# Kernel optimization log

Hardware: AMD Instinct MI355X
Metric: run time of the kernel (lower is better)

The kernel has to match this reference:

```python
import jax, jax.numpy as jnp
import numpy as np

NUM_HEAD = 8
DIM_MODEL = 512
DIM_HEAD = DIM_MODEL // NUM_HEAD
LN_EPS = 1e-5


def setup_inputs() -> dict:
    key = jax.random.key(0)
    ks = jax.random.split(key, 12)
    B, L, D = 4, 2048, DIM_MODEL
    s = 0.02
    return {
        "x": jax.random.normal(ks[0], (B, L, D), dtype=jnp.float32),
        "Wq": jax.random.normal(ks[1], (D, D), dtype=jnp.float32) * s,
        "bq": jnp.zeros((D,), dtype=jnp.float32),
        "Wk": jax.random.normal(ks[2], (D, D), dtype=jnp.float32) * s,
        "bk": jnp.zeros((D,), dtype=jnp.float32),
        "Wv": jax.random.normal(ks[3], (D, D), dtype=jnp.float32) * s,
        "bv": jnp.zeros((D,), dtype=jnp.float32),
        "Wo": jax.random.normal(ks[4], (D, D), dtype=jnp.float32) * s,
        "bo": jnp.zeros((D,), dtype=jnp.float32),
        "gamma": jnp.ones((D,), dtype=jnp.float32),
        "beta": jnp.zeros((D,), dtype=jnp.float32),
    }


def reference(x, Wq, bq, Wk, bk, Wv, bv, Wo, bo, gamma, beta):
    B, L, D = x.shape
    H, dh = NUM_HEAD, D // NUM_HEAD
    # QKV projections (torch Linear: x @ W.T + b)
    Q = x @ Wq.T + bq
    K = x @ Wk.T + bk
    V = x @ Wv.T + bv
    # Faithful to the torch code: contiguous view(B*H, L, dh)
    Q = Q.reshape(B * H, L, dh)
    K = K.reshape(B * H, L, dh)
    V = V.reshape(B * H, L, dh)
    scale = dh ** (-0.5)
    # [B*H, L, L] scores, scaled, softmax over keys
    attn = jax.nn.softmax(jnp.einsum("bqd,bkd->bqk", Q, K) * scale, axis=-1)
    context = jnp.einsum("bqk,bkd->bqd", attn, V)  # [B*H, L, dh]
    context = context.reshape(B, L, D)
    out = context @ Wo.T + bo
    out = out + x  # residual (dropout p=0.0 -> identity)
    # LayerNorm over last dim
    mu = jnp.mean(out, axis=-1, keepdims=True)
    var = jnp.mean(jnp.square(out - mu), axis=-1, keepdims=True)
    out = (out - mu) / jnp.sqrt(var + LN_EPS) * gamma + beta
    return out
```

## Files before the change

### kernel.cpp

```cpp
#include <hip/hip_runtime.h>

typedef __bf16 bf16;
typedef __bf16 bf16x4 __attribute__((ext_vector_type(4)));
typedef __bf16 bf16x8 __attribute__((ext_vector_type(8)));
typedef float f32x4 __attribute__((ext_vector_type(4)));
typedef float f32x16 __attribute__((ext_vector_type(16)));
typedef unsigned int u32;

#define MFMA16(A, B, C) __builtin_amdgcn_mfma_f32_16x16x32_bf16((A), (B), (C), 0, 0, 0)
#define MFMA32(A, B, C) __builtin_amdgcn_mfma_f32_32x32x16_bf16((A), (B), (C), 0, 0, 0)

constexpr int Dm   = 512;
constexpr int Lm   = 2048;
constexpr int DH   = 64;
constexpr int Mrows = 8192;
constexpr int NHEADS = 32;

__device__ __forceinline__ void gload16(const void* g, void* l) {
    __builtin_amdgcn_global_load_lds(
        (const __attribute__((address_space(1))) void*)g,
        (__attribute__((address_space(3))) void*)l, 16, 0, 0);
}

__device__ __forceinline__ u32 pack2(float a, float b) {
    unsigned short la = __builtin_bit_cast(unsigned short, (bf16)a);
    unsigned short lb = __builtin_bit_cast(unsigned short, (bf16)b);
    return (u32)la | ((u32)lb << 16);
}

__global__ __launch_bounds__(256)
void cvt_kernel(const float* __restrict__ x, const float* __restrict__ Wq,
                const float* __restrict__ Wk, const float* __restrict__ Wv,
                const float* __restrict__ Wo,
                bf16* __restrict__ xb, bf16* __restrict__ Wqb, bf16* __restrict__ Wkb,
                bf16* __restrict__ Wvb, bf16* __restrict__ Wob)
{
    size_t i = ((size_t)blockIdx.x * 256 + threadIdx.x) * 4;
    const float* src; bf16* dst; size_t off;
    if (i < (size_t)Mrows * Dm) {
        src = x; dst = xb; off = i;
    } else {
        size_t r = i - (size_t)Mrows * Dm;
        int w = (int)(r >> 18);
        off = r & 262143;
        src = (w == 0) ? Wq : (w == 1) ? Wk : (w == 2) ? Wv : Wo;
        dst = (w == 0) ? Wqb : (w == 1) ? Wkb : (w == 2) ? Wvb : Wob;
    }
    float4 v = *reinterpret_cast<const float4*>(src + off);
    bf16x4 o; o[0] = (bf16)v.x; o[1] = (bf16)v.y; o[2] = (bf16)v.z; o[3] = (bf16)v.w;
    *reinterpret_cast<bf16x4*>(dst + off) = o;
}

__global__ __launch_bounds__(256)
void qkv_gemm(const bf16* __restrict__ xb,
              const bf16* __restrict__ Wqb, const float* __restrict__ bq,
              const bf16* __restrict__ Wkb, const float* __restrict__ bk,
              const bf16* __restrict__ Wvb, const float* __restrict__ bv,
              bf16* __restrict__ Qo, bf16* __restrict__ Ko, bf16* __restrict__ Vo)
{
    __shared__ bf16 Asm[128 * 64];
    __shared__ bf16 Bsm[128 * 64];

    const int z = blockIdx.z;
    const bf16* W = (z == 0) ? Wqb : (z == 1) ? Wkb : Wvb;
    const float* bias = (z == 0) ? bq : (z == 1) ? bk : bv;
    bf16* out = (z == 0) ? Qo : (z == 1) ? Ko : Vo;

    const int tid = threadIdx.x;
    const int row0 = blockIdx.y * 128;
    const int col0 = blockIdx.x * 128;

    const int wv = tid >> 6;
    const int ln = tid & 63;
    const int wr = wv >> 1, wc = wv & 1;
    const int lr = ln & 15;
    const int lg = ln >> 4;

    const int srow_b = wv * 8 + (ln >> 3);
    const int ssc = ((ln & 7) ^ (ln >> 3)) * 8;

    f32x4 acc[4][4] = {};

    for (int kt = 0; kt < Dm; kt += 64) {
        __syncthreads();
        #pragma unroll
        for (int j = 0; j < 4; ++j) {
            const int row = j * 32 + srow_b;
            const int base = (j * 256 + wv * 64) * 8;
            gload16(xb + (size_t)(row0 + row) * Dm + kt + ssc, &Asm[base]);
            gload16(W + (size_t)(col0 + row) * Dm + kt + ssc, &Bsm[base]);
        }
        __syncthreads();

        #pragma unroll
        for (int ks = 0; ks < 2; ++ks) {
            bf16x8 af[4], bfv[4];
            #pragma unroll
            for (int m = 0; m < 4; ++m) {
                const int R = wr * 64 + m * 16 + lr;
                af[m] = *reinterpret_cast<const bf16x8*>(&Asm[R * 64 + (((ks * 4 + lg) ^ (R & 7)) * 8)]);
            }
            #pragma unroll
            for (int n = 0; n < 4; ++n) {
                const int R = wc * 64 + n * 16 + lr;
                bfv[n] = *reinterpret_cast<const bf16x8*>(&Bsm[R * 64 + (((ks * 4 + lg) ^ (R & 7)) * 8)]);
            }
            #pragma unroll
            for (int m = 0; m < 4; ++m)
                #pragma unroll
                for (int n = 0; n < 4; ++n)
                    acc[m][n] = MFMA16(af[m], bfv[n], acc[m][n]);
        }
    }

    #pragma unroll
    for (int m = 0; m < 4; ++m)
        #pragma unroll
        for (int n = 0; n < 4; ++n)
            #pragma unroll
            for (int i = 0; i < 4; ++i) {
                int r = row0 + wr * 64 + m * 16 + lg * 4 + i;
                int c = col0 + wc * 64 + n * 16 + lr;
                out[(size_t)r * Dm + c] = (bf16)(acc[m][n][i] + bias[c]);
            }
}

__global__ __launch_bounds__(256)
void oproj_gemm(const bf16* __restrict__ ctx, const bf16* __restrict__ Wob,
                const float* __restrict__ bo, const float* __restrict__ x,
                float* __restrict__ tmp)
{
    __shared__ bf16 Asm[128 * 64];
    __shared__ bf16 Bsm[128 * 64];

    const int tid = threadIdx.x;
    const int row0 = blockIdx.y * 128;
    const int col0 = blockIdx.x * 128;

    const int wv = tid >> 6;
    const int ln = tid & 63;
    const int wr = wv >> 1, wc = wv & 1;
    const int lr = ln & 15;
    const int lg = ln >> 4;

    const int srow_b = wv * 8 + (ln >> 3);
    const int ssc = ((ln & 7) ^ (ln >> 3)) * 8;

    f32x4 acc[4][4] = {};

    for (int kt = 0; kt < Dm; kt += 64) {
        __syncthreads();
        #pragma unroll
        for (int j = 0; j < 4; ++j) {
            const int row = j * 32 + srow_b;
            const int base = (j * 256 + wv * 64) * 8;
            gload16(ctx + (size_t)(row0 + row) * Dm + kt + ssc, &Asm[base]);
            gload16(Wob + (size_t)(col0 + row) * Dm + kt + ssc, &Bsm[base]);
        }
        __syncthreads();

        #pragma unroll
        for (int ks = 0; ks < 2; ++ks) {
            bf16x8 af[4], bfv[4];
            #pragma unroll
            for (int m = 0; m < 4; ++m) {
                const int R = wr * 64 + m * 16 + lr;
                af[m] = *reinterpret_cast<const bf16x8*>(&Asm[R * 64 + (((ks * 4 + lg) ^ (R & 7)) * 8)]);
            }
            #pragma unroll
            for (int n = 0; n < 4; ++n) {
                const int R = wc * 64 + n * 16 + lr;
                bfv[n] = *reinterpret_cast<const bf16x8*>(&Bsm[R * 64 + (((ks * 4 + lg) ^ (R & 7)) * 8)]);
            }
            #pragma unroll
            for (int m = 0; m < 4; ++m)
                #pragma unroll
                for (int n = 0; n < 4; ++n)
                    acc[m][n] = MFMA16(af[m], bfv[n], acc[m][n]);
        }
    }

    #pragma unroll
    for (int m = 0; m < 4; ++m)
        #pragma unroll
        for (int n = 0; n < 4; ++n)
            #pragma unroll
            for (int i = 0; i < 4; ++i) {
                int r = row0 + wr * 64 + m * 16 + lg * 4 + i;
                int c = col0 + wc * 64 + n * 16 + lr;
                tmp[(size_t)r * Dm + c] = acc[m][n][i] + bo[c] + x[(size_t)r * Dm + c];
            }
}

__global__ __launch_bounds__(256)
void vt_kernel(const bf16* __restrict__ V, bf16* __restrict__ Vt)
{
    __shared__ bf16 T[64 * 72];
    const int head = blockIdx.y;
    const int k0 = blockIdx.x * 64;
    const size_t hb = (size_t)head * (Lm * DH);
    const int tid = threadIdx.x;
    const int r = tid >> 2;
    const int seg = (tid & 3) * 16;

    {
        const bf16* src = &V[hb + (size_t)(k0 + r) * DH + seg];
        *reinterpret_cast<bf16x8*>(&T[r * 72 + seg])     = reinterpret_cast<const bf16x8*>(src)[0];
        *reinterpret_cast<bf16x8*>(&T[r * 72 + seg + 8]) = reinterpret_cast<const bf16x8*>(src)[1];
    }
    __syncthreads();
    bf16 o[16];
    #pragma unroll
    for (int j = 0; j < 16; ++j) o[j] = T[(seg + j) * 72 + r];
    *reinterpret_cast<bf16x8*>(&Vt[hb + (size_t)r * Lm + k0 + seg])     = *reinterpret_cast<bf16x8*>(&o[0]);
    *reinterpret_cast<bf16x8*>(&Vt[hb + (size_t)r * Lm + k0 + seg + 8]) = *reinterpret_cast<bf16x8*>(&o[8]);
}

__global__ __launch_bounds__(512)
void flash_attn(const bf16* __restrict__ Q, const bf16* __restrict__ K,
                const bf16* __restrict__ Vt, bf16* __restrict__ ctx)
{
    __shared__ bf16 Ksm[2][64 * 76];
    __shared__ bf16 Vsm[2][64 * 76];

    const int head = blockIdx.y;
    const int q0 = blockIdx.x * 256;
    const size_t hb = (size_t)head * (Lm * DH);

    const int tid = threadIdx.x;
    const int wv = tid >> 6;
    const int ln = tid & 63;
    const int q31 = ln & 31;
    const int hi = ln >> 5;

    const int srow = tid >> 3;
    const int scu  = tid & 7;
    const int sb = srow * 76 + scu * 8;

    const int qrow = q0 + wv * 32 + q31;

    const float qscale = 0.125f * 1.44269504088896340736f;
    bf16x8 qf[4];
    #pragma unroll
    for (int c = 0; c < 4; ++c) {
        bf16x8 t = *reinterpret_cast<const bf16x8*>(&Q[hb + (size_t)qrow * DH + c * 16 + hi * 8]);
        #pragma unroll
        for (int j = 0; j < 8; ++j) qf[c][j] = (bf16)((float)t[j] * qscale);
    }

    f32x16 acc0 = {};
    f32x16 acc1 = {};
    float lsum = 0.f;

    const bf16* Kp = &K[hb + (size_t)srow * DH + scu * 8];
    const bf16* Vp = &Vt[hb + (size_t)srow * Lm + scu * 8];

    bf16x8 kreg = *reinterpret_cast<const bf16x8*>(Kp);
    bf16x8 vreg = *reinterpret_cast<const bf16x8*>(Vp);
    *reinterpret_cast<bf16x8*>(&Ksm[0][sb]) = kreg;
    *reinterpret_cast<bf16x8*>(&Vsm[0][sb]) = vreg;
    kreg = *reinterpret_cast<const bf16x8*>(Kp + 64 * DH);
    vreg = *reinterpret_cast<const bf16x8*>(Vp + 64);
    __syncthreads();

    constexpr int NT = Lm / 64;
    for (int t = 0; t < NT; ++t) {
        const int cur = t & 1;
        if (t + 1 < NT) {
            *reinterpret_cast<bf16x8*>(&Ksm[cur ^ 1][sb]) = kreg;
            *reinterpret_cast<bf16x8*>(&Vsm[cur ^ 1][sb]) = vreg;
        }
        if (t + 2 < NT) {
            kreg = *reinterpret_cast<const bf16x8*>(Kp + (size_t)(t + 2) * 64 * DH);
            vreg = *reinterpret_cast<const bf16x8*>(Vp + (t + 2) * 64);
        }

        #pragma unroll
        for (int kb = 0; kb < 2; ++kb) {
            f32x16 s = {};
            __builtin_amdgcn_s_setprio(1);
            #pragma unroll
            for (int c = 0; c < 4; ++c) {
                bf16x8 kf = *reinterpret_cast<const bf16x8*>(
                    &Ksm[cur][(kb * 32 + q31) * 76 + (c * 2 + hi) * 8]);
                s = MFMA32(kf, qf[c], s);
            }
            __builtin_amdgcn_s_setprio(0);

            float p[16];
            #pragma unroll
            for (int r = 0; r < 16; ++r) { p[r] = exp2f(s[r]); lsum += p[r]; }

            u32 pk_[8], xk[8];
            #pragma unroll
            for (int r = 0; r < 8; ++r) pk_[r] = pack2(p[2 * r], p[2 * r + 1]);
            #pragma unroll
            for (int r = 0; r < 8; ++r) xk[r] = (u32)__shfl_xor((int)pk_[r], 32);

            union PFrag { u32 w[4]; bf16x8 v; } f0, f1;
            f0.w[0] = hi ? xk[2] : pk_[0];
            f0.w[1] = hi ? xk[3] : pk_[1];
            f0.w[2] = hi ? pk_[2] : xk[0];
            f0.w[3] = hi ? pk_[3] : xk[1];
            f1.w[0] = hi ? xk[6] : pk_[4];
            f1.w[1] = hi ? xk[7] : pk_[5];
            f1.w[2] = hi ? pk_[6] : xk[4];
            f1.w[3] = hi ? pk_[7] : xk[5];

            __builtin_amdgcn_s_setprio(1);
            {
                bf16x8 v00 = *reinterpret_cast<const bf16x8*>(
                    &Vsm[cur][(q31) * 76 + (kb * 4 + hi) * 8]);
                acc0 = MFMA32(v00, f0.v, acc0);
                bf16x8 v01 = *reinterpret_cast<const bf16x8*>(
                    &Vsm[cur][(q31) * 76 + (kb * 4 + 2 + hi) * 8]);
                acc0 = MFMA32(v01, f1.v, acc0);
                bf16x8 v10 = *reinterpret_cast<const bf16x8*>(
                    &Vsm[cur][(32 + q31) * 76 + (kb * 4 + hi) * 8]);
                acc1 = MFMA32(v10, f0.v, acc1);
                bf16x8 v11 = *reinterpret_cast<const bf16x8*>(
                    &Vsm[cur][(32 + q31) * 76 + (kb * 4 + 2 + hi) * 8]);
                acc1 = MFMA32(v11, f1.v, acc1);
            }
            __builtin_amdgcn_s_setprio(0);
        }

        __syncthreads();
    }

    lsum += __shfl_xor(lsum, 32);
    const float inv = 1.f / lsum;

    #pragma unroll
    for (int g8 = 0; g8 < 4; ++g8) {
        bf16x4 o0, o1;
        #pragma unroll
        for (int i = 0; i < 4; ++i) {
            o0[i] = (bf16)(acc0[g8 * 4 + i] * inv);
            o1[i] = (bf16)(acc1[g8 * 4 + i] * inv);
        }
        const int d0 = g8 * 8 + hi * 4;
        *reinterpret_cast<bf16x4*>(&ctx[hb + (size_t)qrow * DH + d0])      = o0;
        *reinterpret_cast<bf16x4*>(&ctx[hb + (size_t)qrow * DH + 32 + d0]) = o1;
    }
}

__global__ __launch_bounds__(128)
void ln_kernel(const float* __restrict__ tmp, const float* __restrict__ gamma,
               const float* __restrict__ beta, float* __restrict__ out)
{
    const int row = blockIdx.x;
    const int tid = threadIdx.x;
    const int wv = tid >> 6;
    const int ln = tid & 63;

    float4 v = reinterpret_cast<const float4*>(tmp + (size_t)row * Dm)[tid];
    float s = v.x + v.y + v.z + v.w;
    float sq = v.x * v.x + v.y * v.y + v.z * v.z + v.w * v.w;

    #pragma unroll
    for (int off = 32; off > 0; off >>= 1) {
        s += __shfl_down(s, off);
        sq += __shfl_down(sq, off);
    }
    __shared__ float red[4];
    if (ln == 0) { red[wv * 2] = s; red[wv * 2 + 1] = sq; }
    __syncthreads();
    s = red[0] + red[2];
    sq = red[1] + red[3];

    const float mu = s * (1.f / Dm);
    const float var = sq * (1.f / Dm) - mu * mu;
    const float rstd = rsqrtf(var + 1e-5f);

    float4 g = reinterpret_cast<const float4*>(gamma)[tid];
    float4 b = reinterpret_cast<const float4*>(beta)[tid];
    float4 o;
    o.x = (v.x - mu) * rstd * g.x + b.x;
    o.y = (v.y - mu) * rstd * g.y + b.y;
    o.z = (v.z - mu) * rstd * g.z + b.z;
    o.w = (v.w - mu) * rstd * g.w + b.w;
    reinterpret_cast<float4*>(out + (size_t)row * Dm)[tid] = o;
}

extern "C" void kernel_launch(void* const* d_in, const int* in_sizes, int n_in,
                              void* d_out, int out_size, void* d_ws, size_t ws_size,
                              hipStream_t stream)
{
    const float* x  = (const float*)d_in[0];
    const float* Wq = (const float*)d_in[1];
    const float* bq = (const float*)d_in[2];
    const float* Wk = (const float*)d_in[3];
    const float* bk = (const float*)d_in[4];
    const float* Wv = (const float*)d_in[5];
    const float* bv = (const float*)d_in[6];
    const float* Wo = (const float*)d_in[7];
    const float* bo = (const float*)d_in[8];
    const float* gamma = (const float*)d_in[9];
    const float* beta  = (const float*)d_in[10];
    float* out = (float*)d_out;

    const size_t MD = (size_t)Mrows * Dm;
    const size_t WD = (size_t)Dm * Dm;
    char* p = (char*)d_ws;
    bf16* xb  = (bf16*)p;                 p += MD * 2;
    bf16* Qw  = (bf16*)p;                 p += MD * 2;
    bf16* Kw  = (bf16*)p;                 p += MD * 2;
    bf16* Vw  = (bf16*)p;                 p += MD * 2;
    bf16* Vtw = (bf16*)p;                 p += MD * 2;
    bf16* Wqb = (bf16*)p;                 p += WD * 2;
    bf16* Wkb = (bf16*)p;                 p += WD * 2;
    bf16* Wvb = (bf16*)p;                 p += WD * 2;
    bf16* Wob = (bf16*)p;                 p += WD * 2;
    float* Tw = (float*)d_ws;
    bf16* Cw = Vw;

    {
        const size_t total = MD + 4 * WD;
        cvt_kernel<<<dim3((unsigned)(total / (256 * 4))), 256, 0, stream>>>(
            x, Wq, Wk, Wv, Wo, xb, Wqb, Wkb, Wvb, Wob);
    }

    qkv_gemm<<<dim3(Dm / 128, Mrows / 128, 3), 256, 0, stream>>>(
        xb, Wqb, bq, Wkb, bk, Wvb, bv, Qw, Kw, Vw);

    vt_kernel<<<dim3(Lm / 64, NHEADS), 256, 0, stream>>>(Vw, Vtw);

    flash_attn<<<dim3(Lm / 256, NHEADS), 512, 0, stream>>>(Qw, Kw, Vtw, Cw);

    oproj_gemm<<<dim3(Dm / 128, Mrows / 128), 256, 0, stream>>>(Cw, Wob, bo, x, Tw);

    ln_kernel<<<dim3(Mrows), 128, 0, stream>>>(Tw, gamma, beta, out);
}
```

Measured before the change: 202.0 us.

## Shrink flash attention blocks, use permlane32 swap, and unroll both key halves

```diff
diff --git a/kernel.cpp b/kernel.cpp
--- a/kernel.cpp
+++ b/kernel.cpp
@@ -26,6 +26,10 @@
     unsigned short la = __builtin_bit_cast(unsigned short, (bf16)a);
     unsigned short lb = __builtin_bit_cast(unsigned short, (bf16)b);
     return (u32)la | ((u32)lb << 16);
+}
+
+__device__ __forceinline__ void pl32swap(u32& a, u32& b) {
+    asm("v_permlane32_swap_b32 %0, %1" : "+v"(a), "+v"(b));
 }
 
 __global__ __launch_bounds__(256)
@@ -216,7 +220,7 @@
     *reinterpret_cast<bf16x8*>(&Vt[hb + (size_t)r * Lm + k0 + seg + 8]) = *reinterpret_cast<bf16x8*>(&o[8]);
 }
 
-__global__ __launch_bounds__(512)
+__global__ __launch_bounds__(256, 2)
 void flash_attn(const bf16* __restrict__ Q, const bf16* __restrict__ K,
                 const bf16* __restrict__ Vt, bf16* __restrict__ ctx)
 {
@@ -224,7 +228,7 @@
     __shared__ bf16 Vsm[2][64 * 76];
 
     const int head = blockIdx.y;
-    const int q0 = blockIdx.x * 256;
+    const int q0 = blockIdx.x * 128;
     const size_t hb = (size_t)head * (Lm * DH);
 
     const int tid = threadIdx.x;
@@ -233,9 +237,9 @@
     const int q31 = ln & 31;
     const int hi = ln >> 5;
 
-    const int srow = tid >> 3;
-    const int scu  = tid & 7;
-    const int sb = srow * 76 + scu * 8;
+    const int srow = tid >> 2;
+    const int scu  = tid & 3;
+    const int sb   = srow * 76 + scu * 8;
 
     const int qrow = q0 + wv * 32 + q31;
 
@@ -255,75 +259,90 @@
     const bf16* Kp = &K[hb + (size_t)srow * DH + scu * 8];
     const bf16* Vp = &Vt[hb + (size_t)srow * Lm + scu * 8];
 
-    bf16x8 kreg = *reinterpret_cast<const bf16x8*>(Kp);
-    bf16x8 vreg = *reinterpret_cast<const bf16x8*>(Vp);
-    *reinterpret_cast<bf16x8*>(&Ksm[0][sb]) = kreg;
-    *reinterpret_cast<bf16x8*>(&Vsm[0][sb]) = vreg;
-    kreg = *reinterpret_cast<const bf16x8*>(Kp + 64 * DH);
-    vreg = *reinterpret_cast<const bf16x8*>(Vp + 64);
+    bf16x8 kr0 = *reinterpret_cast<const bf16x8*>(Kp);
+    bf16x8 kr1 = *reinterpret_cast<const bf16x8*>(Kp + 32);
+    bf16x8 vr0 = *reinterpret_cast<const bf16x8*>(Vp);
+    bf16x8 vr1 = *reinterpret_cast<const bf16x8*>(Vp + 32);
+    *reinterpret_cast<bf16x8*>(&Ksm[0][sb])      = kr0;
+    *reinterpret_cast<bf16x8*>(&Ksm[0][sb + 32]) = kr1;
+    *reinterpret_cast<bf16x8*>(&Vsm[0][sb])      = vr0;
+    *reinterpret_cast<bf16x8*>(&Vsm[0][sb + 32]) = vr1;
+    kr0 = *reinterpret_cast<const bf16x8*>(Kp + 64 * DH);
+    kr1 = *reinterpret_cast<const bf16x8*>(Kp + 64 * DH + 32);
+    vr0 = *reinterpret_cast<const bf16x8*>(Vp + 64);
+    vr1 = *reinterpret_cast<const bf16x8*>(Vp + 64 + 32);
     __syncthreads();
 
     constexpr int NT = Lm / 64;
     for (int t = 0; t < NT; ++t) {
         const int cur = t & 1;
         if (t + 1 < NT) {
-            *reinterpret_cast<bf16x8*>(&Ksm[cur ^ 1][sb]) = kreg;
-            *reinterpret_cast<bf16x8*>(&Vsm[cur ^ 1][sb]) = vreg;
+            *reinterpret_cast<bf16x8*>(&Ksm[cur ^ 1][sb])      = kr0;
+            *reinterpret_cast<bf16x8*>(&Ksm[cur ^ 1][sb + 32]) = kr1;
+            *reinterpret_cast<bf16x8*>(&Vsm[cur ^ 1][sb])      = vr0;
+            *reinterpret_cast<bf16x8*>(&Vsm[cur ^ 1][sb + 32]) = vr1;
         }
         if (t + 2 < NT) {
-            kreg = *reinterpret_cast<const bf16x8*>(Kp + (size_t)(t + 2) * 64 * DH);
-            vreg = *reinterpret_cast<const bf16x8*>(Vp + (t + 2) * 64);
-        }
-
-        #pragma unroll
-        for (int kb = 0; kb < 2; ++kb) {
-            f32x16 s = {};
-            __builtin_amdgcn_s_setprio(1);
-            #pragma unroll
-            for (int c = 0; c < 4; ++c) {
-                bf16x8 kf = *reinterpret_cast<const bf16x8*>(
-                    &Ksm[cur][(kb * 32 + q31) * 76 + (c * 2 + hi) * 8]);
-                s = MFMA32(kf, qf[c], s);
-            }
-            __builtin_amdgcn_s_setprio(0);
-
-            float p[16];
-            #pragma unroll
-            for (int r = 0; r < 16; ++r) { p[r] = exp2f(s[r]); lsum += p[r]; }
-
-            u32 pk_[8], xk[8];
-            #pragma unroll
-            for (int r = 0; r < 8; ++r) pk_[r] = pack2(p[2 * r], p[2 * r + 1]);
-            #pragma unroll
-            for (int r = 0; r < 8; ++r) xk[r] = (u32)__shfl_xor((int)pk_[r], 32);
-
-            union PFrag { u32 w[4]; bf16x8 v; } f0, f1;
-            f0.w[0] = hi ? xk[2] : pk_[0];
-            f0.w[1] = hi ? xk[3] : pk_[1];
-            f0.w[2] = hi ? pk_[2] : xk[0];
-            f0.w[3] = hi ? pk_[3] : xk[1];
-            f1.w[0] = hi ? xk[6] : pk_[4];
-            f1.w[1] = hi ? xk[7] : pk_[5];
-            f1.w[2] = hi ? pk_[6] : xk[4];
-            f1.w[3] = hi ? pk_[7] : xk[5];
-
-            __builtin_amdgcn_s_setprio(1);
-            {
-                bf16x8 v00 = *reinterpret_cast<const bf16x8*>(
-                    &Vsm[cur][(q31) * 76 + (kb * 4 + hi) * 8]);
-                acc0 = MFMA32(v00, f0.v, acc0);
-                bf16x8 v01 = *reinterpret_cast<const bf16x8*>(
-                    &Vsm[cur][(q31) * 76 + (kb * 4 + 2 + hi) * 8]);
-                acc0 = MFMA32(v01, f1.v, acc0);
-                bf16x8 v10 = *reinterpret_cast<const bf16x8*>(
-                    &Vsm[cur][(32 + q31) * 76 + (kb * 4 + hi) * 8]);
-                acc1 = MFMA32(v10, f0.v, acc1);
-                bf16x8 v11 = *reinterpret_cast<const bf16x8*>(
-                    &Vsm[cur][(32 + q31) * 76 + (kb * 4 + 2 + hi) * 8]);
-                acc1 = MFMA32(v11, f1.v, acc1);
-            }
-            __builtin_amdgcn_s_setprio(0);
-        }
+            kr0 = *reinterpret_cast<const bf16x8*>(Kp + (size_t)(t + 2) * 64 * DH);
+            kr1 = *reinterpret_cast<const bf16x8*>(Kp + (size_t)(t + 2) * 64 * DH + 32);
+            vr0 = *reinterpret_cast<const bf16x8*>(Vp + (t + 2) * 64);
+            vr1 = *reinterpret_cast<const bf16x8*>(Vp + (t + 2) * 64 + 32);
+        }
+
+        f32x16 s0 = {}, s1 = {};
+        __builtin_amdgcn_s_setprio(1);
+        #pragma unroll
+        for (int c = 0; c < 4; ++c) {
+            bf16x8 k0 = *reinterpret_cast<const bf16x8*>(&Ksm[cur][(q31) * 76 + (c * 2 + hi) * 8]);
+            s0 = MFMA32(k0, qf[c], s0);
+            bf16x8 k1 = *reinterpret_cast<const bf16x8*>(&Ksm[cur][(32 + q31) * 76 + (c * 2 + hi) * 8]);
+            s1 = MFMA32(k1, qf[c], s1);
+        }
+        __builtin_amdgcn_s_setprio(0);
+
+        float p0[16], p1[16];
+        #pragma unroll
+        for (int r = 0; r < 16; ++r) { p0[r] = exp2f(s0[r]); lsum += p0[r]; }
+        #pragma unroll
+        for (int r = 0; r < 16; ++r) { p1[r] = exp2f(s1[r]); lsum += p1[r]; }
+
+        u32 a0[8], a1[8];
+        #pragma unroll
+        for (int r = 0; r < 8; ++r) a0[r] = pack2(p0[2 * r], p0[2 * r + 1]);
+        #pragma unroll
+        for (int r = 0; r < 8; ++r) a1[r] = pack2(p1[2 * r], p1[2 * r + 1]);
+        pl32swap(a0[0], a0[2]); pl32swap(a0[1], a0[3]);
+        pl32swap(a0[4], a0[6]); pl32swap(a0[5], a0[7]);
+        pl32swap(a1[0], a1[2]); pl32swap(a1[1], a1[3]);
+        pl32swap(a1[4], a1[6]); pl32swap(a1[5], a1[7]);
+
+        union PF { u32 w[4]; bf16x8 v; } f0, f1, f2, f3;
+        f0.w[0] = a0[0]; f0.w[1] = a0[1]; f0.w[2] = a0[2]; f0.w[3] = a0[3];
+        f1.w[0] = a0[4]; f1.w[1] = a0[5]; f1.w[2] = a0[6]; f1.w[3] = a0[7];
+        f2.w[0] = a1[0]; f2.w[1] = a1[1]; f2.w[2] = a1[2]; f2.w[3] = a1[3];
+        f3.w[0] = a1[4]; f3.w[1] = a1[5]; f3.w[2] = a1[6]; f3.w[3] = a1[7];
+
+        __builtin_amdgcn_s_setprio(1);
+        {
+            bf16x8 v;
+            v = *reinterpret_cast<const bf16x8*>(&Vsm[cur][(q31) * 76 + (hi) * 8]);
+            acc0 = MFMA32(v, f0.v, acc0);
+            v = *reinterpret_cast<const bf16x8*>(&Vsm[cur][(q31) * 76 + (2 + hi) * 8]);
+            acc0 = MFMA32(v, f1.v, acc0);
+            v = *reinterpret_cast<const bf16x8*>(&Vsm[cur][(q31) * 76 + (4 + hi) * 8]);
+            acc0 = MFMA32(v, f2.v, acc0);
+            v = *reinterpret_cast<const bf16x8*>(&Vsm[cur][(q31) * 76 + (6 + hi) * 8]);
+            acc0 = MFMA32(v, f3.v, acc0);
+            v = *reinterpret_cast<const bf16x8*>(&Vsm[cur][(32 + q31) * 76 + (hi) * 8]);
+            acc1 = MFMA32(v, f0.v, acc1);
+            v = *reinterpret_cast<const bf16x8*>(&Vsm[cur][(32 + q31) * 76 + (2 + hi) * 8]);
+            acc1 = MFMA32(v, f1.v, acc1);
+            v = *reinterpret_cast<const bf16x8*>(&Vsm[cur][(32 + q31) * 76 + (4 + hi) * 8]);
+            acc1 = MFMA32(v, f2.v, acc1);
+            v = *reinterpret_cast<const bf16x8*>(&Vsm[cur][(32 + q31) * 76 + (6 + hi) * 8]);
+            acc1 = MFMA32(v, f3.v, acc1);
+        }
+        __builtin_amdgcn_s_setprio(0);
 
         __syncthreads();
     }
@@ -426,7 +445,7 @@
 
     vt_kernel<<<dim3(Lm / 64, NHEADS), 256, 0, stream>>>(Vw, Vtw);
 
-    flash_attn<<<dim3(Lm / 256, NHEADS), 512, 0, stream>>>(Qw, Kw, Vtw, Cw);
+    flash_attn<<<dim3(Lm / 128, NHEADS), 256, 0, stream>>>(Qw, Kw, Vtw, Cw);
 
     oproj_gemm<<<dim3(Dm / 128, Mrows / 128), 256, 0, stream>>>(Cw, Wob, bo, x, Tw);
 
```

After: 203.1 us. About the same (+0.6%).
